# Optimization experiments

Measured on AMD Instinct MI355X. Metric: run time of the kernel, lower is better.

## Reference

```python
import jax, jax.numpy as jnp
import numpy as np

N, E = 50000, 500000
IN_C, HID, OUT_C, HEADS, NL = 128, 16, 16, 8, 4
EPS = 1e-5
NEG_SLOPE = 0.2


def _gatv2(x, src, dst, Wl, Wr, att, bias, concat):
    # GATv2Conv (PyG semantics, eval mode): lin_l on source, lin_r on target,
    # e = a . LeakyReLU(xl[src] + xr[dst]); segment softmax over dst; scatter-sum.
    n = x.shape[0]
    H, C = att.shape
    xl = (x @ Wl).reshape(n, H, C)
    xr = (x @ Wr).reshape(n, H, C)
    e = jax.nn.leaky_relu(xl[src] + xr[dst], NEG_SLOPE)          # [E', H, C]
    logit = jnp.einsum('ehc,hc->eh', e, att)                      # [E', H]
    mx = jax.lax.stop_gradient(jax.ops.segment_max(logit, dst, num_segments=n))
    a = jnp.exp(logit - mx[dst])
    denom = jax.ops.segment_sum(a, dst, num_segments=n)
    alpha = a / denom[dst]                                        # [E', H]
    out = jax.ops.segment_sum(xl[src] * alpha[..., None], dst, num_segments=n)
    out = out.reshape(n, H * C) if concat else out.mean(axis=1)
    return out + bias


def _bn_eval(x, g, b, m, v):
    return (x - m) * jax.lax.rsqrt(v + EPS) * g + b


def setup_inputs() -> dict:
    key = jax.random.key(0)
    ks = jax.random.split(key, 32)
    d = {}
    d['x'] = jax.random.normal(ks[0], (N, IN_C), dtype=jnp.float32)
    d['edge_index'] = jax.random.randint(ks[1], (2, E), 0, N, dtype=jnp.int64)
    HC = HID * HEADS  # 128
    dims_in = [IN_C, HC, HC, HC]
    dims_h = [HEADS, HEADS, HEADS, 1]
    dims_c = [HID, HID, HID, OUT_C]
    ki = 2
    for i in range(NL):
        fan = dims_in[i]
        s = 1.0 / np.sqrt(fan)
        d[f'W{i}l'] = jax.random.uniform(ks[ki], (fan, dims_h[i] * dims_c[i]), minval=-s, maxval=s, dtype=jnp.float32); ki += 1
        d[f'W{i}r'] = jax.random.uniform(ks[ki], (fan, dims_h[i] * dims_c[i]), minval=-s, maxval=s, dtype=jnp.float32); ki += 1
        d[f'a{i}'] = jax.random.normal(ks[ki], (dims_h[i], dims_c[i]), dtype=jnp.float32) * 0.1; ki += 1
        out_dim = dims_h[i] * dims_c[i] if i < NL - 1 else dims_c[i]
        d[f'b{i}'] = jnp.zeros((out_dim,), dtype=jnp.float32)
    for i in range(NL - 1):
        d[f'g{i}'] = jnp.ones((HC,), dtype=jnp.float32) + 0.1 * jax.random.normal(ks[ki], (HC,), dtype=jnp.float32); ki += 1
        d[f'be{i}'] = 0.1 * jax.random.normal(ks[ki], (HC,), dtype=jnp.float32); ki += 1
        d[f'm{i}'] = 0.1 * jax.random.normal(ks[ki], (HC,), dtype=jnp.float32); ki += 1
        d[f'v{i}'] = jnp.ones((HC,), dtype=jnp.float32)
    return d


def reference(x, edge_index, W0l, W0r, a0, b0, W1l, W1r, a1, b1, W2l, W2r, a2, b2, W3l, W3r, a3, b3, g0, be0, m0, v0, g1, be1, m1, v1, g2, be2, m2, v2):
    n = x.shape[0]
    loop = jnp.arange(n, dtype=edge_index.dtype)
    src = jnp.concatenate([edge_index[0], loop])  # add_self_loops=True (PyG default)
    dst = jnp.concatenate([edge_index[1], loop])
    Ws = [(W0l, W0r, a0, b0), (W1l, W1r, a1, b1), (W2l, W2r, a2, b2), (W3l, W3r, a3, b3)]
    bns = [(g0, be0, m0, v0), (g1, be1, m1, v1), (g2, be2, m2, v2)]
    h = x
    for i in range(NL):
        Wl, Wr, att, bias = Ws[i]
        h = _gatv2(h, src, dst, Wl, Wr, att, bias, concat=(i < NL - 1))
        if i < NL - 1:
            g, b, m, v = bns[i]
            h = jax.nn.elu(_bn_eval(h, g, b, m, v))
    return h
```

## Files before the change

### kernel.cpp

```cpp
#include <hip/hip_runtime.h>
#include <hip/hip_fp16.h>
#include <math.h>

static constexpr float BN_EPS = 1e-5f;
static constexpr float NEG = 0.2f;

typedef float f32x4 __attribute__((ext_vector_type(4)));
typedef _Float16 h16x2 __attribute__((ext_vector_type(2)));
typedef _Float16 h16x8 __attribute__((ext_vector_type(8)));


__global__ __launch_bounds__(256) void hist_pack(
    const int* __restrict__ ei, int E, int n, int* __restrict__ cnt,
    const float* __restrict__ W0l, const float* __restrict__ W0r,
    const float* __restrict__ W1l, const float* __restrict__ W1r,
    const float* __restrict__ W2l, const float* __restrict__ W2r,
    const float* __restrict__ W3l, const float* __restrict__ W3r,
    __half* __restrict__ pk0, __half* __restrict__ pk1,
    __half* __restrict__ pk2, __half* __restrict__ pk3,
    const float* __restrict__ b0, const float* __restrict__ b1,
    const float* __restrict__ b2,
    const float* __restrict__ g0, const float* __restrict__ g1,
    const float* __restrict__ g2,
    const float* __restrict__ be0, const float* __restrict__ be1,
    const float* __restrict__ be2,
    const float* __restrict__ m0, const float* __restrict__ m1,
    const float* __restrict__ m2,
    const float* __restrict__ v0, const float* __restrict__ v1,
    const float* __restrict__ v2,
    float* __restrict__ bnA, float* __restrict__ bnB) {
    int b = blockIdx.x;
    if (b < 200) {
        if (threadIdx.x >= 64) return;
        const float *Wl, *Wr;
        __half* packed;
        int tile, NTT, M;
        if (b < 192) {
            int layer = b >> 6;
            tile = b & 63;
            NTT = 16; M = 128;
            Wl = (layer == 0) ? W0l : (layer == 1) ? W1l : W2l;
            Wr = (layer == 0) ? W0r : (layer == 1) ? W1r : W2r;
            packed = (layer == 0) ? pk0 : (layer == 1) ? pk1 : pk2;
        } else {
            tile = b - 192;
            NTT = 2; M = 16;
            Wl = W3l; Wr = W3r; packed = pk3;
        }
        int NT = NTT >> 1;
        int gnt = tile % NTT;
        int kt = tile / NTT;
        int l = threadIdx.x;
        const float* W = (gnt < NT) ? Wl : Wr;
        int col = (gnt % NT) * 16 + (l & 15);
        int krow = kt * 32 + ((l >> 4) << 3);
        size_t base = (size_t)tile * 512 + (size_t)l * 8;
#pragma unroll
        for (int j = 0; j < 8; j++)
            packed[base + j] = __float2half(W[(size_t)(krow + j) * M + col]);
    } else if (b == 200) {
        for (int t = threadIdx.x; t < 384; t += 256) {
            int layer = t >> 7;
            int c = t & 127;
            const float* gg = (layer == 0) ? g0 : (layer == 1) ? g1 : g2;
            const float* ee = (layer == 0) ? be0 : (layer == 1) ? be1 : be2;
            const float* mm = (layer == 0) ? m0 : (layer == 1) ? m1 : m2;
            const float* vv = (layer == 0) ? v0 : (layer == 1) ? v1 : v2;
            const float* bb = (layer == 0) ? b0 : (layer == 1) ? b1 : b2;
            float A = gg[c] * rsqrtf(vv[c] + BN_EPS);
            bnA[t] = A;
            bnB[t] = fmaf(bb[c] - mm[c], A, ee[c]);
        }
    } else {
        int e = (b - 201) * 256 + threadIdx.x;
        int ET = E + n;
        if (e >= ET) return;
        int d = (e < E) ? ei[E + e] : (e - E);
        atomicAdd(&cnt[d], 1);
    }
}


__device__ __forceinline__ void scan_block_body256(
    const int* __restrict__ cnt, int* __restrict__ rowptr,
    int* __restrict__ bsums, int n, int bid, int* s) {
    int t = threadIdx.x;
    int base = bid * 1024 + t * 4;
    int v0 = 0, v1 = 0, v2 = 0, v3 = 0;
    if (base + 3 < n) {
        v0 = cnt[base];     v1 = cnt[base + 1];
        v2 = cnt[base + 2]; v3 = cnt[base + 3];
    } else {
        if (base < n)     v0 = cnt[base];
        if (base + 1 < n) v1 = cnt[base + 1];
        if (base + 2 < n) v2 = cnt[base + 2];
        if (base + 3 < n) v3 = cnt[base + 3];
    }
    int p1 = v0 + v1, p2 = p1 + v2, p3 = p2 + v3;
    s[t] = p3;
    __syncthreads();
    for (int d = 1; d < 256; d <<= 1) {
        int tt = (t >= d) ? s[t - d] : 0;
        __syncthreads();
        s[t] += tt;
        __syncthreads();
    }
    int ex = s[t] - p3;
    if (base < n)     rowptr[base + 1] = ex + v0;
    if (base + 1 < n) rowptr[base + 2] = ex + p1;
    if (base + 2 < n) rowptr[base + 3] = ex + p2;
    if (base + 3 < n) rowptr[base + 4] = ex + p3;
    if (t == 255) bsums[bid] = s[255];
}

__global__ __launch_bounds__(256) void scatfin(
    const int* __restrict__ ei, int E, int n,
    const int* __restrict__ rowraw, const int* __restrict__ bsums, int nb,
    int* __restrict__ fill, int* __restrict__ col, int* __restrict__ rowfin,
    int nbF) {
    __shared__ int spre[64];
    if (threadIdx.x < 64) {
        int L = threadIdx.x;
        int bv = (L < nb) ? bsums[L] : 0;
#pragma unroll
        for (int d = 1; d < 64; d <<= 1) {
            int t = __shfl_up(bv, d);
            if (L >= d) bv += t;
        }
        int ex = __shfl_up(bv, 1);
        if (L == 0) ex = 0;
        spre[L] = ex;
    }
    __syncthreads();
    int b = blockIdx.x;
    if (b < nbF) {
        int i0 = b * 1024 + threadIdx.x * 4;
#pragma unroll
        for (int j = 0; j < 4; j++) {
            int i = i0 + j;
            if (i < n) rowfin[i + 1] = rowraw[i + 1] + spre[i >> 10];
        }
        if (b == 0 && threadIdx.x == 0) rowfin[0] = 0;
    } else {
        int e = (b - nbF) * 256 + threadIdx.x;
        int ET = E + n;
        if (e >= ET) return;
        int s, d;
        if (e < E) { s = ei[e]; d = ei[E + e]; } else { s = e - E; d = s; }
        int pos = atomicAdd(&fill[d], 1);
        int base = (d == 0) ? 0 : (rowraw[d] + spre[(d - 1) >> 10]);
        col[base + pos] = s;
    }
}


template <bool FIRST>
__device__ __forceinline__ void gemm_body(
    const __half* __restrict__ xh, const float* __restrict__ xf,
    const __half* __restrict__ packed,
    __half* __restrict__ Y1, __half* __restrict__ Y2, int n, int bid,
    _Float16* sA) {
    const int t = threadIdx.x;
    const int row0 = bid * 64;

    for (int c = t; c < 1024; c += 256) {
        int row = c >> 4;
        int off = (c & 15) * 8;
        int gr = row0 + row;
        if (gr >= n) gr = n - 1;
        if (FIRST) {
            float4 v0 = *(const float4*)&xf[(size_t)gr * 128 + off];
            float4 v1 = *(const float4*)&xf[(size_t)gr * 128 + off + 4];
            h16x8 h = {(_Float16)v0.x, (_Float16)v0.y, (_Float16)v0.z, (_Float16)v0.w,
                       (_Float16)v1.x, (_Float16)v1.y, (_Float16)v1.z, (_Float16)v1.w};
            *(h16x8*)&sA[row * 136 + off] = h;
        } else {
            *(h16x8*)&sA[row * 136 + off] = *(const h16x8*)&xh[(size_t)gr * 128 + off];
        }
    }
    __syncthreads();

    const int lane = t & 63;
    const int s = t >> 6;
    const int lr = lane & 15;
    const int kq = (lane >> 4) * 8;

    h16x8 af[4][4];
#pragma unroll
    for (int rt = 0; rt < 4; rt++)
#pragma unroll
        for (int kt = 0; kt < 4; kt++)
            af[rt][kt] = *(const h16x8*)&sA[(rt * 16 + lr) * 136 + kt * 32 + kq];

    f32x4 acc[4][4];
#pragma unroll
    for (int a = 0; a < 4; a++)
#pragma unroll
        for (int b = 0; b < 4; b++) acc[a][b] = (f32x4){0.f, 0.f, 0.f, 0.f};

#pragma unroll
    for (int kt = 0; kt < 4; kt++) {
#pragma unroll
        for (int ntl = 0; ntl < 4; ntl++) {
            int nt = s * 4 + ntl;
            h16x8 b = *(const h16x8*)&packed[((size_t)(kt * 16 + nt)) * 512 + lane * 8];
#pragma unroll
            for (int rt = 0; rt < 4; rt++)
                acc[ntl][rt] = __builtin_amdgcn_mfma_f32_16x16x32_f16(b, af[rt][kt], acc[ntl][rt], 0, 0, 0);
        }
    }

    __half* Y = (s < 2) ? Y1 : Y2;
    const int colh = (s & 1) * 64;
    const int rq = (lane >> 4) * 4;
#pragma unroll
    for (int rt = 0; rt < 4; rt++) {
        int row = row0 + rt * 16 + lr;
        if (row >= n) continue;
#pragma unroll
        for (int ntl = 0; ntl < 4; ntl++) {
            int c0 = colh + ntl * 16 + rq;
            ushort4 o = make_ushort4(
                __half_as_ushort(__float2half(acc[ntl][rt][0])),
                __half_as_ushort(__float2half(acc[ntl][rt][1])),
                __half_as_ushort(__float2half(acc[ntl][rt][2])),
                __half_as_ushort(__float2half(acc[ntl][rt][3])));
            *(ushort4*)&Y[(size_t)row * 128 + c0] = o;
        }
    }
}

__global__ __launch_bounds__(256) void gemm_h_big2(
    const __half* __restrict__ xh, const __half* __restrict__ packed,
    __half* __restrict__ Y1, __half* __restrict__ Y2, int n) {
    __shared__ __align__(16) char smem[64 * 136 * 2];
    gemm_body<false>(xh, nullptr, packed, Y1, Y2, n, blockIdx.x, (_Float16*)smem);
}

__global__ __launch_bounds__(256) void scanblk_gemm0(
    const int* __restrict__ cnt, int* __restrict__ rowraw,
    int* __restrict__ bsums, int n, int nscan,
    const float* __restrict__ xf, const __half* __restrict__ packed,
    __half* __restrict__ Y1, __half* __restrict__ Y2) {
    __shared__ __align__(16) char smem[64 * 136 * 2];
    int b = blockIdx.x;
    if (b < nscan) {
        scan_block_body256(cnt, rowraw, bsums, n, b, (int*)smem);
    } else {
        gemm_body<true>(nullptr, xf, packed, Y1, Y2, n, b - nscan,
                        (_Float16*)smem);
    }
}


__global__ __launch_bounds__(256) void gemm_h_small(
    const __half* __restrict__ xh, const __half* __restrict__ packed,
    float* __restrict__ Y1, float* __restrict__ Y2, int n) {
    int lane = threadIdx.x & 63;
    int wv = blockIdx.x * 4 + (threadIdx.x >> 6);
    int row0 = wv * 16;
    if (row0 >= n) return;
    int r = row0 + (lane & 15);
    int rl = (r >= n) ? (n - 1) : r;
    int kq = (lane >> 4) * 8;

    h16x8 af[4];
#pragma unroll
    for (int kt = 0; kt < 4; kt++)
        af[kt] = *(const h16x8*)&xh[(size_t)rl * 128 + kt * 32 + kq];

    f32x4 acc[2];
    acc[0] = (f32x4){0.f, 0.f, 0.f, 0.f};
    acc[1] = (f32x4){0.f, 0.f, 0.f, 0.f};

#pragma unroll
    for (int kt = 0; kt < 4; kt++) {
#pragma unroll
        for (int nt = 0; nt < 2; nt++) {
            h16x8 b = *(const h16x8*)&packed[((size_t)(kt * 2 + nt)) * 512 + lane * 8];
            acc[nt] = __builtin_amdgcn_mfma_f32_16x16x32_f16(b, af[kt], acc[nt], 0, 0, 0);
        }
    }

    if (r < n) {
        int rq = (lane >> 4) * 4;
#pragma unroll
        for (int nt = 0; nt < 2; nt++) {
            float* Y = (nt == 0) ? Y1 : Y2;
            *(float4*)&Y[(size_t)r * 16 + rq] =
                make_float4(acc[nt][0], acc[nt][1], acc[nt][2], acc[nt][3]);
        }
    }
}


__device__ __forceinline__ float dot8_h(const h16x2* lp, const h16x2* ap) {
#if __has_builtin(__builtin_amdgcn_fdot2)
    float part = __builtin_amdgcn_fdot2(lp[0], ap[0], 0.f, false);
    part = __builtin_amdgcn_fdot2(lp[1], ap[1], part, false);
    part = __builtin_amdgcn_fdot2(lp[2], ap[2], part, false);
    return __builtin_amdgcn_fdot2(lp[3], ap[3], part, false);
#else
    float part = 0.f;
#pragma unroll
    for (int i = 0; i < 4; i++)
        part += (float)lp[i].x * (float)ap[i].x + (float)lp[i].y * (float)ap[i].y;
    return part;
#endif
}

__global__ __launch_bounds__(256) void agg_h(
    const __half* __restrict__ xl, const __half* __restrict__ xr,
    const int* __restrict__ rowptr, const int* __restrict__ col,
    const float* __restrict__ att,
    const float* __restrict__ bnA, const float* __restrict__ bnB,
    __half* __restrict__ oh, int n) {
    int v = (blockIdx.x * blockDim.x + threadIdx.x) >> 4;
    if (v >= n) return;
    int L = threadIdx.x & 15;
    int ch = L * 8;

    int beg = rowptr[v];
    int end = rowptr[v + 1];
    int cb = beg;
    int cidx = (cb + L < end) ? col[cb + L] : v;

    h16x8 rx = *(const h16x8*)&xr[((size_t)v << 7) + ch];
    float4 av0 = *(const float4*)&att[ch];
    float4 av1 = *(const float4*)&att[ch + 4];
    h16x2 a[4] = {{(_Float16)av0.x, (_Float16)av0.y},
                  {(_Float16)av0.z, (_Float16)av0.w},
                  {(_Float16)av1.x, (_Float16)av1.y},
                  {(_Float16)av1.z, (_Float16)av1.w}};
    const h16x8 neg8 = {(_Float16)NEG, (_Float16)NEG, (_Float16)NEG, (_Float16)NEG,
                        (_Float16)NEG, (_Float16)NEG, (_Float16)NEG, (_Float16)NEG};

    float lrun = 0.f;
    float acc[8] = {0.f, 0.f, 0.f, 0.f, 0.f, 0.f, 0.f, 0.f};

    auto proc = [&](h16x8 hv, bool ok) {
        h16x8 s = hv + rx;
        h16x8 l = __builtin_elementwise_max(s, s * neg8);
        const h16x2* lp = (const h16x2*)&l;
        float part = dot8_h(lp, a);
        part += __shfl_xor(part, 1);
        float p = ok ? __expf(part) : 0.f;
        lrun += p;
        const _Float16* hp = (const _Float16*)&hv;
#pragma unroll
        for (int k = 0; k < 8; k++) acc[k] = fmaf(p, (float)hp[k], acc[k]);
    };

    while (true) {
        int ce = min(end, cb + 16);
        for (int e = cb; e < ce; e += 8) {
            int off = e - cb;
            h16x8 hv[8];
#pragma unroll
            for (int j = 0; j < 8; j++) {
                int u = __shfl(cidx, off + j, 16);
                hv[j] = *(const h16x8*)&xl[((size_t)u << 7) + ch];
            }
#pragma unroll
            for (int j = 0; j < 8; j++) proc(hv[j], e + j < end);
        }
        cb += 16;
        if (cb >= end) break;
        cidx = (cb + L < end) ? col[cb + L] : v;
    }

    float inv = 1.0f / lrun;
    float4 A0 = *(const float4*)&bnA[ch];
    float4 A1 = *(const float4*)&bnA[ch + 4];
    float4 B0 = *(const float4*)&bnB[ch];
    float4 B1 = *(const float4*)&bnB[ch + 4];
    float Av[8] = {A0.x, A0.y, A0.z, A0.w, A1.x, A1.y, A1.z, A1.w};
    float Bv[8] = {B0.x, B0.y, B0.z, B0.w, B1.x, B1.y, B1.z, B1.w};
    h16x8 outv;
#pragma unroll
    for (int k = 0; k < 8; k++) {
        float o = fmaf(acc[k], inv * Av[k], Bv[k]);
        o = o > 0.f ? o : expm1f(o);
        outv[k] = (_Float16)o;
    }
    *(h16x8*)&oh[((size_t)v << 7) + ch] = outv;
}


__global__ __launch_bounds__(256) void agg_f(
    const float* __restrict__ xl, const float* __restrict__ xr,
    const int* __restrict__ rowptr, const int* __restrict__ col,
    const float* __restrict__ att, const float* __restrict__ bias,
    float* __restrict__ out, int n) {
    int v = (blockIdx.x * blockDim.x + threadIdx.x) >> 2;
    if (v >= n) return;
    int L = threadIdx.x & 3;
    int ch = 4 * L;

    int beg = rowptr[v];
    int end = rowptr[v + 1];
    int cb = beg;
    int cidx = (cb + L < end) ? col[cb + L] : v;

    float4 xrv = *(const float4*)&xr[((size_t)v << 4) + ch];
    float4 av = *(const float4*)&att[ch];

    float lrun = 0.f;
    float4 acc = make_float4(0.f, 0.f, 0.f, 0.f);

    while (true) {
        float4 xv[4];
#pragma unroll
        for (int j = 0; j < 4; j++) {
            int u = __shfl(cidx, j, 4);
            xv[j] = *(const float4*)&xl[((size_t)u << 4) + ch];
        }
#pragma unroll
        for (int j = 0; j < 4; j++) {
            bool ok = (cb + j < end);
            float s0 = xv[j].x + xrv.x; s0 = s0 > 0.f ? s0 : NEG * s0;
            float s1 = xv[j].y + xrv.y; s1 = s1 > 0.f ? s1 : NEG * s1;
            float s2 = xv[j].z + xrv.z; s2 = s2 > 0.f ? s2 : NEG * s2;
            float s3 = xv[j].w + xrv.w; s3 = s3 > 0.f ? s3 : NEG * s3;
            float part = fmaf(s0, av.x, fmaf(s1, av.y, fmaf(s2, av.z, s3 * av.w)));
            part += __shfl_xor(part, 1);
            part += __shfl_xor(part, 2);
            float p = ok ? __expf(part) : 0.f;
            lrun += p;
            acc.x = fmaf(p, xv[j].x, acc.x);
            acc.y = fmaf(p, xv[j].y, acc.y);
            acc.z = fmaf(p, xv[j].z, acc.z);
            acc.w = fmaf(p, xv[j].w, acc.w);
        }
        cb += 4;
        if (cb >= end) break;
        cidx = (cb + L < end) ? col[cb + L] : v;
    }

    float inv = 1.0f / lrun;
    float4 b4 = *(const float4*)&bias[ch];
    *(float4*)&out[((size_t)v << 4) + ch] =
        make_float4(fmaf(acc.x, inv, b4.x), fmaf(acc.y, inv, b4.y),
                    fmaf(acc.z, inv, b4.z), fmaf(acc.w, inv, b4.w));
}


extern "C" void kernel_launch(void* const* d_in, const int* in_sizes, int n_in,
                              void* d_out, int out_size, void* d_ws, size_t ws_size,
                              hipStream_t stream) {
    const float* x = (const float*)d_in[0];
    const int* ei = (const int*)d_in[1];
    const float* Wl[4] = {(const float*)d_in[2], (const float*)d_in[6],
                          (const float*)d_in[10], (const float*)d_in[14]};
    const float* Wr[4] = {(const float*)d_in[3], (const float*)d_in[7],
                          (const float*)d_in[11], (const float*)d_in[15]};
    const float* att[4] = {(const float*)d_in[4], (const float*)d_in[8],
                           (const float*)d_in[12], (const float*)d_in[16]};
    const float* bias[4] = {(const float*)d_in[5], (const float*)d_in[9],
                            (const float*)d_in[13], (const float*)d_in[17]};
    const float* g[3] = {(const float*)d_in[18], (const float*)d_in[22], (const float*)d_in[26]};
    const float* be[3] = {(const float*)d_in[19], (const float*)d_in[23], (const float*)d_in[27]};
    const float* bm[3] = {(const float*)d_in[20], (const float*)d_in[24], (const float*)d_in[28]};
    const float* bv[3] = {(const float*)d_in[21], (const float*)d_in[25], (const float*)d_in[29]};

    const int n = in_sizes[0] / 128;
    const int E = in_sizes[1] / 2;
    const int ET = E + n;

    char* p = (char*)d_ws;
    __half* xh = (__half*)p;           p += (size_t)n * 128 * 2;
    __half* xlh = (__half*)p;          p += (size_t)n * 128 * 2;
    __half* xrh = (__half*)p;          p += (size_t)n * 128 * 2;
    float* xl3 = (float*)p;            p += (size_t)n * 16 * 4;
    float* xr3 = (float*)p;            p += (size_t)n * 16 * 4;
    int* rowraw = (int*)p;            p += (size_t)(n + 4) * 4;
    int* rowfin = (int*)p;            p += (size_t)(n + 4) * 4;
    int* cnt = (int*)p;               p += (size_t)n * 4;
    int* fill = (int*)p;              p += (size_t)n * 4;
    int* col = (int*)p;               p += (size_t)ET * 4;
    int* bsums = (int*)p;             p += 256;
    __half* pk[4];
    for (int i = 0; i < 3; i++) { pk[i] = (__half*)p; p += 4 * 16 * 512 * 2; }
    pk[3] = (__half*)p;               p += 4 * 2 * 512 * 2;
    float* bnA = (float*)p;           p += 384 * 4;
    float* bnB = (float*)p;           p += 384 * 4;

    (void)hipMemsetAsync(cnt, 0, (size_t)n * 8, stream);

    const int tb = 256;
    const int histBlocks = (ET + tb - 1) / tb;
    hist_pack<<<201 + histBlocks, tb, 0, stream>>>(
        ei, E, n, cnt,
        Wl[0], Wr[0], Wl[1], Wr[1], Wl[2], Wr[2], Wl[3], Wr[3],
        pk[0], pk[1], pk[2], pk[3],
        bias[0], bias[1], bias[2],
        g[0], g[1], g[2], be[0], be[1], be[2],
        bm[0], bm[1], bm[2], bv[0], bv[1], bv[2],
        bnA, bnB);

    const int nb = (n + 1023) / 1024;
    const int gb64 = (n + 63) / 64;
    const int gemmBlocksSmall = ((n + 15) / 16 + 3) / 4;
    const int aggBlocksH = (n + 15) / 16;
    const int aggBlocksF = (n + 63) / 64;

    scanblk_gemm0<<<nb + gb64, 256, 0, stream>>>(
        cnt, rowraw, bsums, n, nb, x, pk[0], xlh, xrh);
    scatfin<<<nb + histBlocks, tb, 0, stream>>>(
        ei, E, n, rowraw, bsums, nb, fill, col, rowfin, nb);

    agg_h<<<aggBlocksH, 256, 0, stream>>>(
        xlh, xrh, rowfin, col, att[0], bnA, bnB, xh, n);
    for (int i = 1; i < 3; i++) {
        gemm_h_big2<<<gb64, 256, 0, stream>>>(xh, pk[i], xlh, xrh, n);
        agg_h<<<aggBlocksH, 256, 0, stream>>>(
            xlh, xrh, rowfin, col, att[i], bnA + 128 * i, bnB + 128 * i, xh, n);
    }
    gemm_h_small<<<gemmBlocksSmall, 256, 0, stream>>>(xh, pk[3], xl3, xr3, n);
    agg_f<<<aggBlocksF, 256, 0, stream>>>(
        xl3, xr3, rowfin, col, att[3], bias[3], (float*)d_out, n);
}
```

Before: 331.4 us.

## Fuse GAT aggregation with next layer's projection GEMM via LDS

Each aggregation kernel now writes its 64-row output tile into LDS and immediately runs the next layer's MFMA projection on it. This removes the intermediate xh buffer round-trip through global memory and three kernel launches. Ping-pong xl/xr buffers avoid read/write hazards between layers. The edge gather batch shrinks from 8 to 4 loads in flight, and each block handles 4 node groups serially, which may reduce memory-level parallelism in the gather phase.

```diff
diff --git a/kernel.cpp b/kernel.cpp
--- a/kernel.cpp
+++ b/kernel.cpp
@@ -154,32 +154,10 @@
 }
 
 
-template <bool FIRST>
-__device__ __forceinline__ void gemm_body(
-    const __half* __restrict__ xh, const float* __restrict__ xf,
-    const __half* __restrict__ packed,
-    __half* __restrict__ Y1, __half* __restrict__ Y2, int n, int bid,
-    _Float16* sA) {
+__device__ __forceinline__ void gemm_compute_from_lds(
+    const _Float16* sA, const __half* __restrict__ packed,
+    __half* __restrict__ Y1, __half* __restrict__ Y2, int n, int row0) {
     const int t = threadIdx.x;
-    const int row0 = bid * 64;
-
-    for (int c = t; c < 1024; c += 256) {
-        int row = c >> 4;
-        int off = (c & 15) * 8;
-        int gr = row0 + row;
-        if (gr >= n) gr = n - 1;
-        if (FIRST) {
-            float4 v0 = *(const float4*)&xf[(size_t)gr * 128 + off];
-            float4 v1 = *(const float4*)&xf[(size_t)gr * 128 + off + 4];
-            h16x8 h = {(_Float16)v0.x, (_Float16)v0.y, (_Float16)v0.z, (_Float16)v0.w,
-                       (_Float16)v1.x, (_Float16)v1.y, (_Float16)v1.z, (_Float16)v1.w};
-            *(h16x8*)&sA[row * 136 + off] = h;
-        } else {
-            *(h16x8*)&sA[row * 136 + off] = *(const h16x8*)&xh[(size_t)gr * 128 + off];
-        }
-    }
-    __syncthreads();
-
     const int lane = t & 63;
     const int s = t >> 6;
     const int lr = lane & 15;
@@ -228,13 +206,6 @@
             *(ushort4*)&Y[(size_t)row * 128 + c0] = o;
         }
     }
-}
-
-__global__ __launch_bounds__(256) void gemm_h_big2(
-    const __half* __restrict__ xh, const __half* __restrict__ packed,
-    __half* __restrict__ Y1, __half* __restrict__ Y2, int n) {
-    __shared__ __align__(16) char smem[64 * 136 * 2];
-    gemm_body<false>(xh, nullptr, packed, Y1, Y2, n, blockIdx.x, (_Float16*)smem);
 }
 
 __global__ __launch_bounds__(256) void scanblk_gemm0(
@@ -246,51 +217,24 @@
     int b = blockIdx.x;
     if (b < nscan) {
         scan_block_body256(cnt, rowraw, bsums, n, b, (int*)smem);
-    } else {
-        gemm_body<true>(nullptr, xf, packed, Y1, Y2, n, b - nscan,
-                        (_Float16*)smem);
-    }
-}
-
-
-__global__ __launch_bounds__(256) void gemm_h_small(
-    const __half* __restrict__ xh, const __half* __restrict__ packed,
-    float* __restrict__ Y1, float* __restrict__ Y2, int n) {
-    int lane = threadIdx.x & 63;
-    int wv = blockIdx.x * 4 + (threadIdx.x >> 6);
-    int row0 = wv * 16;
-    if (row0 >= n) return;
-    int r = row0 + (lane & 15);
-    int rl = (r >= n) ? (n - 1) : r;
-    int kq = (lane >> 4) * 8;
-
-    h16x8 af[4];
-#pragma unroll
-    for (int kt = 0; kt < 4; kt++)
-        af[kt] = *(const h16x8*)&xh[(size_t)rl * 128 + kt * 32 + kq];
-
-    f32x4 acc[2];
-    acc[0] = (f32x4){0.f, 0.f, 0.f, 0.f};
-    acc[1] = (f32x4){0.f, 0.f, 0.f, 0.f};
-
-#pragma unroll
-    for (int kt = 0; kt < 4; kt++) {
-#pragma unroll
-        for (int nt = 0; nt < 2; nt++) {
-            h16x8 b = *(const h16x8*)&packed[((size_t)(kt * 2 + nt)) * 512 + lane * 8];
-            acc[nt] = __builtin_amdgcn_mfma_f32_16x16x32_f16(b, af[kt], acc[nt], 0, 0, 0);
-        }
-    }
-
-    if (r < n) {
-        int rq = (lane >> 4) * 4;
-#pragma unroll
-        for (int nt = 0; nt < 2; nt++) {
-            float* Y = (nt == 0) ? Y1 : Y2;
-            *(float4*)&Y[(size_t)r * 16 + rq] =
-                make_float4(acc[nt][0], acc[nt][1], acc[nt][2], acc[nt][3]);
-        }
-    }
+        return;
+    }
+    _Float16* sA = (_Float16*)smem;
+    int bid = b - nscan;
+    int row0 = bid * 64;
+    for (int c = threadIdx.x; c < 1024; c += 256) {
+        int row = c >> 4;
+        int off = (c & 15) * 8;
+        int gr = row0 + row;
+        if (gr >= n) gr = n - 1;
+        float4 v0 = *(const float4*)&xf[(size_t)gr * 128 + off];
+        float4 v1 = *(const float4*)&xf[(size_t)gr * 128 + off + 4];
+        h16x8 h = {(_Float16)v0.x, (_Float16)v0.y, (_Float16)v0.z, (_Float16)v0.w,
+                   (_Float16)v1.x, (_Float16)v1.y, (_Float16)v1.z, (_Float16)v1.w};
+        *(h16x8*)&sA[row * 136 + off] = h;
+    }
+    __syncthreads();
+    gemm_compute_from_lds(sA, packed, Y1, Y2, n, row0);
 }
 
 
@@ -309,16 +253,18 @@
 #endif
 }
 
-__global__ __launch_bounds__(256) void agg_h(
+__device__ __forceinline__ void agg_node_to_lds(
     const __half* __restrict__ xl, const __half* __restrict__ xr,
     const int* __restrict__ rowptr, const int* __restrict__ col,
     const float* __restrict__ att,
     const float* __restrict__ bnA, const float* __restrict__ bnB,
-    __half* __restrict__ oh, int n) {
-    int v = (blockIdx.x * blockDim.x + threadIdx.x) >> 4;
-    if (v >= n) return;
-    int L = threadIdx.x & 15;
+    _Float16* sA, int v, int rowLocal, int L, int n) {
     int ch = L * 8;
+    if (v >= n) {
+        h16x8 z = {};
+        *(h16x8*)&sA[rowLocal * 136 + ch] = z;
+        return;
+    }
 
     int beg = rowptr[v];
     int end = rowptr[v + 1];
@@ -353,16 +299,16 @@
 
     while (true) {
         int ce = min(end, cb + 16);
-        for (int e = cb; e < ce; e += 8) {
+        for (int e = cb; e < ce; e += 4) {
             int off = e - cb;
-            h16x8 hv[8];
-#pragma unroll
-            for (int j = 0; j < 8; j++) {
+            h16x8 hv[4];
+#pragma unroll
+            for (int j = 0; j < 4; j++) {
                 int u = __shfl(cidx, off + j, 16);
                 hv[j] = *(const h16x8*)&xl[((size_t)u << 7) + ch];
             }
 #pragma unroll
-            for (int j = 0; j < 8; j++) proc(hv[j], e + j < end);
+            for (int j = 0; j < 4; j++) proc(hv[j], e + j < end);
         }
         cb += 16;
         if (cb >= end) break;
@@ -383,7 +329,70 @@
         o = o > 0.f ? o : expm1f(o);
         outv[k] = (_Float16)o;
     }
-    *(h16x8*)&oh[((size_t)v << 7) + ch] = outv;
+    *(h16x8*)&sA[rowLocal * 136 + ch] = outv;
+}
+
+
+template <bool SMALL>
+__global__ __launch_bounds__(256) void agg_gemm(
+    const __half* __restrict__ xl, const __half* __restrict__ xr,
+    const int* __restrict__ rowptr, const int* __restrict__ col,
+    const float* __restrict__ att,
+    const float* __restrict__ bnA, const float* __restrict__ bnB,
+    const __half* __restrict__ packed,
+    __half* __restrict__ Y1, __half* __restrict__ Y2,
+    float* __restrict__ F1, float* __restrict__ F2, int n) {
+    __shared__ __align__(16) _Float16 sA[64 * 136];
+    const int t = threadIdx.x;
+    const int row0 = blockIdx.x * 64;
+    const int L = t & 15;
+    const int grp = t >> 4;
+
+#pragma unroll
+    for (int sub = 0; sub < 4; sub++) {
+        int rowLocal = sub * 16 + grp;
+        agg_node_to_lds(xl, xr, rowptr, col, att, bnA, bnB,
+                        sA, row0 + rowLocal, rowLocal, L, n);
+    }
+    __syncthreads();
+
+    if (!SMALL) {
+        gemm_compute_from_lds(sA, packed, Y1, Y2, n, row0);
+    } else {
+        int lane = t & 63;
+        int s = t >> 6;
+        int rloc = s * 16 + (lane & 15);
+        int r = row0 + rloc;
+        int kq = (lane >> 4) * 8;
+
+        h16x8 af[4];
+#pragma unroll
+        for (int kt = 0; kt < 4; kt++)
+            af[kt] = *(const h16x8*)&sA[rloc * 136 + kt * 32 + kq];
+
+        f32x4 acc[2];
+        acc[0] = (f32x4){0.f, 0.f, 0.f, 0.f};
+        acc[1] = (f32x4){0.f, 0.f, 0.f, 0.f};
+
+#pragma unroll
+        for (int kt = 0; kt < 4; kt++) {
+#pragma unroll
+            for (int nt = 0; nt < 2; nt++) {
+                h16x8 b = *(const h16x8*)&packed[((size_t)(kt * 2 + nt)) * 512 + lane * 8];
+                acc[nt] = __builtin_amdgcn_mfma_f32_16x16x32_f16(b, af[kt], acc[nt], 0, 0, 0);
+            }
+        }
+
+        if (r < n) {
+            int rq = (lane >> 4) * 4;
+#pragma unroll
+            for (int nt = 0; nt < 2; nt++) {
+                float* Y = (nt == 0) ? F1 : F2;
+                *(float4*)&Y[(size_t)r * 16 + rq] =
+                    make_float4(acc[nt][0], acc[nt][1], acc[nt][2], acc[nt][3]);
+            }
+        }
+    }
 }
 
 
@@ -468,9 +477,10 @@
     const int ET = E + n;
 
     char* p = (char*)d_ws;
-    __half* xh = (__half*)p;           p += (size_t)n * 128 * 2;
-    __half* xlh = (__half*)p;          p += (size_t)n * 128 * 2;
-    __half* xrh = (__half*)p;          p += (size_t)n * 128 * 2;
+    __half* xlA = (__half*)p;          p += (size_t)n * 128 * 2;
+    __half* xrA = (__half*)p;          p += (size_t)n * 128 * 2;
+    __half* xlB = (__half*)p;          p += (size_t)n * 128 * 2;
+    __half* xrB = (__half*)p;          p += (size_t)n * 128 * 2;
     float* xl3 = (float*)p;            p += (size_t)n * 16 * 4;
     float* xr3 = (float*)p;            p += (size_t)n * 16 * 4;
     int* rowraw = (int*)p;            p += (size_t)(n + 4) * 4;
@@ -500,23 +510,23 @@
 
     const int nb = (n + 1023) / 1024;
     const int gb64 = (n + 63) / 64;
-    const int gemmBlocksSmall = ((n + 15) / 16 + 3) / 4;
-    const int aggBlocksH = (n + 15) / 16;
     const int aggBlocksF = (n + 63) / 64;
 
     scanblk_gemm0<<<nb + gb64, 256, 0, stream>>>(
-        cnt, rowraw, bsums, n, nb, x, pk[0], xlh, xrh);
+        cnt, rowraw, bsums, n, nb, x, pk[0], xlA, xrA);
     scatfin<<<nb + histBlocks, tb, 0, stream>>>(
         ei, E, n, rowraw, bsums, nb, fill, col, rowfin, nb);
 
-    agg_h<<<aggBlocksH, 256, 0, stream>>>(
-        xlh, xrh, rowfin, col, att[0], bnA, bnB, xh, n);
-    for (int i = 1; i < 3; i++) {
-        gemm_h_big2<<<gb64, 256, 0, stream>>>(xh, pk[i], xlh, xrh, n);
-        agg_h<<<aggBlocksH, 256, 0, stream>>>(
-            xlh, xrh, rowfin, col, att[i], bnA + 128 * i, bnB + 128 * i, xh, n);
-    }
-    gemm_h_small<<<gemmBlocksSmall, 256, 0, stream>>>(xh, pk[3], xl3, xr3, n);
+    agg_gemm<false><<<gb64, 256, 0, stream>>>(
+        xlA, xrA, rowfin, col, att[0], bnA, bnB, pk[1],
+        xlB, xrB, nullptr, nullptr, n);
+    agg_gemm<false><<<gb64, 256, 0, stream>>>(
+        xlB, xrB, rowfin, col, att[1], bnA + 128, bnB + 128, pk[2],
+        xlA, xrA, nullptr, nullptr, n);
+    agg_gemm<true><<<gb64, 256, 0, stream>>>(
+        xlA, xrA, rowfin, col, att[2], bnA + 256, bnB + 256, pk[3],
+        nullptr, nullptr, xl3, xr3, n);
+
     agg_f<<<aggBlocksF, 256, 0, stream>>>(
         xl3, xr3, rowfin, col, att[3], bias[3], (float*)d_out, n);
 }
```

Measured after the change: 344.4 us. 1.04x slower.
